# Optimization experiments

Hardware: AMD Instinct MI355X
Metric: run time of the kernel (lower is better)

The kernel has to match this reference:

```python
import jax, jax.numpy as jnp
import numpy as np

N_NODES = 100000
N_EDGES = 1600000
IN_DIM, HID_DIM, OUT_DIM = 512, 128, 64


def setup_inputs() -> dict:
    key = jax.random.key(0)
    k1, k2, k3, k4, k5, k6 = jax.random.split(key, 6)
    feature = jax.random.normal(k1, (N_NODES, IN_DIM), dtype=jnp.float32)
    edge_row = jax.random.randint(k2, (N_EDGES,), 0, N_NODES, dtype=jnp.int32)
    edge_col = jax.random.randint(k3, (N_EDGES,), 0, N_NODES, dtype=jnp.int32)
    edge_vals = jax.random.uniform(k4, (N_EDGES,), dtype=jnp.float32)
    W1 = jax.random.normal(k5, (IN_DIM, HID_DIM), dtype=jnp.float32) * (IN_DIM ** -0.5)
    W2 = jax.random.normal(k6, (HID_DIM, OUT_DIM), dtype=jnp.float32) * (HID_DIM ** -0.5)
    return {"feature": feature, "edge_row": edge_row, "edge_col": edge_col,
            "edge_vals": edge_vals, "W1": W1, "W2": W2}


def spmm(edge_row, edge_col, edge_vals, dense):
    # sparse [N,N] @ dense [N,D]: out[r] += v * dense[c] for each edge (r,c,v)
    gathered = edge_vals[:, None] * dense[edge_col]  # [E, D]
    return jax.ops.segment_sum(gathered, edge_row, num_segments=N_NODES)


def reference(feature, edge_row, edge_col, edge_vals, W1, W2):
    # layer 1: support = X @ W1; h = relu(A @ support)
    h = jax.nn.relu(spmm(edge_row, edge_col, edge_vals, feature @ W1))
    # layer 2: logits = A @ (h @ W2)
    logits = spmm(edge_row, edge_col, edge_vals, h @ W2)
    return logits
```

## Files before the change

### kernel.cpp

```cpp
#include <hip/hip_runtime.h>

#define N_NODES 100000
#define N_EDGES 1600000
#define IN_DIM 512
#define HID_DIM 128
#define OUT_DIM 64

typedef __attribute__((ext_vector_type(8))) short bf16x8;
typedef __attribute__((ext_vector_type(4))) float f32x4;

__device__ __forceinline__ unsigned int f2bf_rne(float f) {
    union { float f; unsigned u; } v; v.f = f;
    unsigned r = v.u + 0x7fffu + ((v.u >> 16) & 1u);
    return r >> 16;
}

__global__ __launch_bounds__(256) void wcvt(const float* __restrict__ W1,
                                            unsigned short* __restrict__ W1t) {
    __shared__ float T[64][65];
    const int bk = blockIdx.x >> 1;
    const int bn = blockIdx.x & 1;
    const int t = threadIdx.x;
#pragma unroll
    for (int i = 0; i < 4; i++) {
        int fi = t + i * 256;
        int kk = fi >> 4;
        int f  = fi & 15;
        float4 v = *(const float4*)&W1[(long)(bk * 64 + kk) * HID_DIM + bn * 64 + f * 4];
        T[kk][f * 4 + 0] = v.x; T[kk][f * 4 + 1] = v.y;
        T[kk][f * 4 + 2] = v.z; T[kk][f * 4 + 3] = v.w;
    }
    __syncthreads();
#pragma unroll
    for (int i = 0; i < 8; i++) {
        int di = t + i * 256;
        int n  = di >> 5;
        int dw = di & 31;
        unsigned lo = f2bf_rne(T[dw * 2 + 0][n]);
        unsigned hi = f2bf_rne(T[dw * 2 + 1][n]);
        unsigned short* dst = W1t + (long)(bn * 64 + n) * IN_DIM + bk * 64 + dw * 2;
        *(unsigned int*)dst = lo | (hi << 16);
    }
}

__global__ __launch_bounds__(256) void wcvt2(const float* __restrict__ W2,
                                             unsigned short* __restrict__ W2t) {
    __shared__ float T[128][65];
    const int t = threadIdx.x;
#pragma unroll
    for (int i = 0; i < 8; i++) {
        int fi = t + i * 256;
        int k = fi >> 4;
        int f = fi & 15;
        float4 v = *(const float4*)&W2[(long)k * OUT_DIM + f * 4];
        T[k][f * 4 + 0] = v.x; T[k][f * 4 + 1] = v.y;
        T[k][f * 4 + 2] = v.z; T[k][f * 4 + 3] = v.w;
    }
    __syncthreads();
#pragma unroll
    for (int i = 0; i < 16; i++) {
        int di = t + i * 256;
        int n  = di >> 6;
        int dw = di & 63;
        unsigned lo = f2bf_rne(T[dw * 2 + 0][n]);
        unsigned hi = f2bf_rne(T[dw * 2 + 1][n]);
        *(unsigned int*)(W2t + (long)n * HID_DIM + dw * 2) = lo | (hi << 16);
    }
}

__global__ __launch_bounds__(256) void gemm1_mfma(const float* __restrict__ X,
                                                  const unsigned short* __restrict__ W1t,
                                                  unsigned short* __restrict__ outb) {
    __shared__ unsigned short As[64][40];
    const int tid  = threadIdx.x;
    const int lane = tid & 63;
    const int w    = tid >> 6;
    const int m    = lane & 15;
    const int hi   = lane >> 4;
    const int rowBase = blockIdx.x * 64;

    f32x4 acc[4][2] = {};

    const int sr = tid >> 2;
    const int sk = (tid & 3) * 8;
    int gr = rowBase + sr;
    if (gr >= N_NODES) gr = N_NODES - 1;
    const float* xp = X + (long)gr * IN_DIM;

    const unsigned short* b0p = W1t + (long)(w * 32 + m) * IN_DIM + hi * 8;
    const unsigned short* b1p = W1t + (long)(w * 32 + 16 + m) * IN_DIM + hi * 8;

    for (int k0 = 0; k0 < IN_DIM; k0 += 32) {
        float4 xa = *(const float4*)(xp + k0 + sk);
        float4 xb = *(const float4*)(xp + k0 + sk + 4);
        uint4 pk;
        pk.x = f2bf_rne(xa.x) | (f2bf_rne(xa.y) << 16);
        pk.y = f2bf_rne(xa.z) | (f2bf_rne(xa.w) << 16);
        pk.z = f2bf_rne(xb.x) | (f2bf_rne(xb.y) << 16);
        pk.w = f2bf_rne(xb.z) | (f2bf_rne(xb.w) << 16);
        *(uint4*)&As[sr][sk] = pk;
        __syncthreads();

        bf16x8 bf0 = *(const bf16x8*)(b0p + k0);
        bf16x8 bf1 = *(const bf16x8*)(b1p + k0);
#pragma unroll
        for (int t = 0; t < 4; t++) {
            bf16x8 af = *(const bf16x8*)&As[t * 16 + m][hi * 8];
            acc[t][0] = __builtin_amdgcn_mfma_f32_16x16x32_bf16(af, bf0, acc[t][0], 0, 0, 0);
            acc[t][1] = __builtin_amdgcn_mfma_f32_16x16x32_bf16(af, bf1, acc[t][1], 0, 0, 0);
        }
        __syncthreads();
    }

#pragma unroll
    for (int t = 0; t < 4; t++) {
#pragma unroll
        for (int r = 0; r < 4; r++) {
            int row = rowBase + t * 16 + hi * 4 + r;
            if (row < N_NODES) {
                outb[(long)row * HID_DIM + w * 32 + m] =
                    (unsigned short)f2bf_rne(acc[t][0][r]);
                outb[(long)row * HID_DIM + w * 32 + 16 + m] =
                    (unsigned short)f2bf_rne(acc[t][1][r]);
            }
        }
    }
}

__global__ __launch_bounds__(256) void gemm2_mfma(const unsigned short* __restrict__ hb,
                                                  const unsigned short* __restrict__ W2t,
                                                  float* __restrict__ hw) {
    const int tid  = threadIdx.x;
    const int lane = tid & 63;
    const int w    = tid >> 6;
    const int m    = lane & 15;
    const int hi   = lane >> 4;
    const long rowBase = (long)blockIdx.x * 128 + w * 32;

    bf16x8 bfrag[4][4];
#pragma unroll
    for (int nt = 0; nt < 4; nt++) {
        const unsigned short* bp = W2t + (long)(nt * 16 + m) * HID_DIM + hi * 8;
#pragma unroll
        for (int ks = 0; ks < 4; ks++)
            bfrag[ks][nt] = *(const bf16x8*)(bp + ks * 32);
    }

    f32x4 acc[2][4] = {};
#pragma unroll
    for (int mt = 0; mt < 2; mt++) {
        long r = rowBase + mt * 16 + m;
        if (r >= N_NODES) r = N_NODES - 1;
        const unsigned short* ap = hb + r * HID_DIM + hi * 8;
#pragma unroll
        for (int ks = 0; ks < 4; ks++) {
            bf16x8 af = *(const bf16x8*)(ap + ks * 32);
#pragma unroll
            for (int nt = 0; nt < 4; nt++)
                acc[mt][nt] = __builtin_amdgcn_mfma_f32_16x16x32_bf16(
                    af, bfrag[ks][nt], acc[mt][nt], 0, 0, 0);
        }
    }

#pragma unroll
    for (int mt = 0; mt < 2; mt++)
#pragma unroll
        for (int nt = 0; nt < 4; nt++)
#pragma unroll
            for (int r = 0; r < 4; r++) {
                long row = rowBase + mt * 16 + hi * 4 + r;
                if (row < N_NODES)
                    hw[row * OUT_DIM + nt * 16 + m] = acc[mt][nt][r];
            }
}

__global__ __launch_bounds__(256) void hist_rows(const int* __restrict__ rows,
                                                 int* __restrict__ cnt) {
    int e = blockIdx.x * 256 + threadIdx.x;
    if (e < N_EDGES) atomicAdd(&cnt[rows[e]], 1);
}

#define SCAN_BLOCKS ((N_NODES + 255) / 256)

__global__ __launch_bounds__(256) void scan_pass1(int* __restrict__ cnt,
                                                  int* __restrict__ bsum) {
    __shared__ int s[256];
    const int t = threadIdx.x;
    const int i = blockIdx.x * 256 + t;
    int v = (i < N_NODES) ? cnt[i] : 0;
    s[t] = v;
    __syncthreads();
    for (int off = 1; off < 256; off <<= 1) {
        int u = (t >= off) ? s[t - off] : 0;
        __syncthreads();
        s[t] += u;
        __syncthreads();
    }
    if (i < N_NODES) cnt[i] = s[t] - v;
    if (t == 255) bsum[blockIdx.x] = s[255];
}

__global__ __launch_bounds__(512) void scan_pass2(int* __restrict__ bsum,
                                                  int* __restrict__ boff) {
    __shared__ int s[512];
    const int t = threadIdx.x;
    int v = (t < SCAN_BLOCKS) ? bsum[t] : 0;
    s[t] = v;
    __syncthreads();
    for (int off = 1; off < 512; off <<= 1) {
        int u = (t >= off) ? s[t - off] : 0;
        __syncthreads();
        s[t] += u;
        __syncthreads();
    }
    if (t < SCAN_BLOCKS) boff[t] = s[t] - v;
}

__global__ __launch_bounds__(256) void scan_pass3(const int* __restrict__ cnt,
                                                  const int* __restrict__ boff,
                                                  int* __restrict__ rowptr,
                                                  int* __restrict__ cursor) {
    const int i = blockIdx.x * 256 + threadIdx.x;
    if (i < N_NODES) {
        int r = cnt[i] + boff[blockIdx.x];
        rowptr[i] = r;
        cursor[i] = r;
    }
    if (i == 0) rowptr[N_NODES] = N_EDGES;
}

__global__ __launch_bounds__(256) void scatter_edges(const int* __restrict__ rows,
                                                     const int* __restrict__ cols,
                                                     const float* __restrict__ vals,
                                                     int* __restrict__ cursor,
                                                     int2* __restrict__ sedge) {
    int e = blockIdx.x * 256 + threadIdx.x;
    if (e < N_EDGES) {
        int p = atomicAdd(&cursor[rows[e]], 1);
        sedge[p] = make_int2(cols[e], __float_as_int(vals[e]));
    }
}

__global__ __launch_bounds__(256) void spmm1(const int* __restrict__ rowptr,
                                             const int2* __restrict__ sedge,
                                             const unsigned short* __restrict__ supb,
                                             unsigned short* __restrict__ outb) {
    const int wid = blockIdx.x * 4 + (threadIdx.x >> 6);
    if (wid >= N_NODES) return;
    const int lane = threadIdx.x & 63;
    const int start = rowptr[wid];
    const int end   = rowptr[wid + 1];

    float accx = 0.f, accy = 0.f;

    for (int base = start; base < end; base += 64) {
        int idx = base + lane;
        int ecol = 0, eval = 0;
        if (idx < end) {
            int2 e = sedge[idx];
            ecol = e.x; eval = e.y;
        }
        const int cnt = min(64, end - base);
        for (int k = 0; k < cnt; k += 8) {
            int   c[8];
            float v[8];
#pragma unroll
            for (int q = 0; q < 8; q++) {
                c[q] = __builtin_amdgcn_readlane(ecol, k + q);
                v[q] = __int_as_float(__builtin_amdgcn_readlane(eval, k + q));
            }
            unsigned u[8];
#pragma unroll
            for (int q = 0; q < 8; q++)
                u[q] = *(const unsigned*)(supb + (long)c[q] * 128 + lane * 2);
#pragma unroll
            for (int q = 0; q < 8; q++) {
                accx += v[q] * __uint_as_float(u[q] << 16);
                accy += v[q] * __uint_as_float(u[q] & 0xffff0000u);
            }
        }
    }

    accx = accx > 0.f ? accx : 0.f;
    accy = accy > 0.f ? accy : 0.f;
    *(unsigned int*)(outb + (long)wid * 128 + lane * 2) =
        f2bf_rne(accx) | (f2bf_rne(accy) << 16);
}

__global__ __launch_bounds__(256) void spmm2(const int* __restrict__ rowptr,
                                             const int2* __restrict__ sedge,
                                             const float* __restrict__ dense,
                                             float* __restrict__ out) {
    const int wid = blockIdx.x * 4 + (threadIdx.x >> 6);
    if (wid >= N_NODES) return;
    const int lane = threadIdx.x & 63;
    const int start = rowptr[wid];
    const int end   = rowptr[wid + 1];

    float acc = 0.f;

    for (int base = start; base < end; base += 64) {
        int idx = base + lane;
        int ecol = 0, eval = 0;
        if (idx < end) {
            int2 e = sedge[idx];
            ecol = e.x; eval = e.y;
        }
        const int cnt = min(64, end - base);
        for (int k = 0; k < cnt; k += 8) {
            int   c[8];
            float v[8];
#pragma unroll
            for (int q = 0; q < 8; q++) {
                c[q] = __builtin_amdgcn_readlane(ecol, k + q);
                v[q] = __int_as_float(__builtin_amdgcn_readlane(eval, k + q));
            }
            float x[8];
#pragma unroll
            for (int q = 0; q < 8; q++)
                x[q] = dense[(long)c[q] * 64 + lane];
#pragma unroll
            for (int q = 0; q < 8; q++)
                acc += v[q] * x[q];
        }
    }

    out[(long)wid * 64 + lane] = acc;
}

extern "C" void kernel_launch(void* const* d_in, const int* in_sizes, int n_in,
                              void* d_out, int out_size, void* d_ws, size_t ws_size,
                              hipStream_t stream) {
    const float* feature = (const float*)d_in[0];
    const int*   erow    = (const int*)d_in[1];
    const int*   ecol    = (const int*)d_in[2];
    const float* evals   = (const float*)d_in[3];
    const float* W1      = (const float*)d_in[4];
    const float* W2      = (const float*)d_in[5];
    float* out = (float*)d_out;

    unsigned short* supb = (unsigned short*)d_ws;
    unsigned short* hb   = supb + (size_t)N_NODES * HID_DIM;
    float* hw      = (float*)(hb + (size_t)N_NODES * HID_DIM);
    int*   cnt     = (int*)(hw + (size_t)N_NODES * OUT_DIM);
    int*   cursor  = cnt + N_NODES;
    int*   rowptr  = cursor + N_NODES;
    int2*  sedge   = (int2*)(rowptr + (N_NODES + 1));
    int*   bsum    = (int*)(sedge + N_EDGES);
    int*   boff    = bsum + SCAN_BLOCKS;
    unsigned short* W1t = (unsigned short*)(boff + SCAN_BLOCKS);
    unsigned short* W2t = W1t + (size_t)HID_DIM * IN_DIM;

    hipMemsetAsync(cnt, 0, (size_t)N_NODES * sizeof(int), stream);
    hist_rows<<<(N_EDGES + 255) / 256, 256, 0, stream>>>(erow, cnt);
    scan_pass1<<<SCAN_BLOCKS, 256, 0, stream>>>(cnt, bsum);
    scan_pass2<<<1, 512, 0, stream>>>(bsum, boff);
    scan_pass3<<<SCAN_BLOCKS, 256, 0, stream>>>(cnt, boff, rowptr, cursor);
    scatter_edges<<<(N_EDGES + 255) / 256, 256, 0, stream>>>(erow, ecol, evals,
                                                             cursor, sedge);

    wcvt<<<16, 256, 0, stream>>>(W1, W1t);
    wcvt2<<<1, 256, 0, stream>>>(W2, W2t);

    gemm1_mfma<<<(N_NODES + 63) / 64, 256, 0, stream>>>(feature, W1t, supb);

    spmm1<<<(N_NODES + 3) / 4, 256, 0, stream>>>(rowptr, sedge, supb, hb);

    gemm2_mfma<<<(N_NODES + 127) / 128, 256, 0, stream>>>(hb, W2t, hw);

    spmm2<<<(N_NODES + 3) / 4, 256, 0, stream>>>(rowptr, sedge, hw, out);
}
```

Baseline: 643.5 us.

## Partition CSR build atomics by XCD row range and widen SpMM gather batches

The histogram and scatter kernels now use a fixed grid where each block's low three index bits pick one of eight row ranges. Each block scans all edges but only does atomics for rows in its range, so atomic traffic for a row range stays on one XCD's L2 rather than spreading across dies. The cost is that every edge's row index is read eight times, using nontemporal loads. Separately, both SpMM kernels unroll the neighbor gather to 16 edges per batch instead of 8, which puts more loads in flight at the cost of more registers.

```diff
diff --git a/kernel.cpp b/kernel.cpp
--- a/kernel.cpp
+++ b/kernel.cpp
@@ -174,10 +174,20 @@
             }
 }
 
-__global__ __launch_bounds__(256) void hist_rows(const int* __restrict__ rows,
-                                                 int* __restrict__ cnt) {
-    int e = blockIdx.x * 256 + threadIdx.x;
-    if (e < N_EDGES) atomicAdd(&cnt[rows[e]], 1);
+#define ROWS_PER_GRP (N_NODES / 8)
+#define CSR_BLOCKS 1024
+
+__global__ __launch_bounds__(256) void hist_xcd(const int* __restrict__ rows,
+                                                int* __restrict__ cnt) {
+    const int grp = blockIdx.x & 7;
+    const int rlo = grp * ROWS_PER_GRP;
+    const int rhi = rlo + ROWS_PER_GRP;
+    const int nb  = gridDim.x >> 3;
+    const int bi  = blockIdx.x >> 3;
+    for (int e = bi * 256 + threadIdx.x; e < N_EDGES; e += nb * 256) {
+        int r = __builtin_nontemporal_load(&rows[e]);
+        if (r >= rlo && r < rhi) atomicAdd(&cnt[r], 1);
+    }
 }
 
 #define SCAN_BLOCKS ((N_NODES + 255) / 256)
@@ -229,15 +239,24 @@
     if (i == 0) rowptr[N_NODES] = N_EDGES;
 }
 
-__global__ __launch_bounds__(256) void scatter_edges(const int* __restrict__ rows,
-                                                     const int* __restrict__ cols,
-                                                     const float* __restrict__ vals,
-                                                     int* __restrict__ cursor,
-                                                     int2* __restrict__ sedge) {
-    int e = blockIdx.x * 256 + threadIdx.x;
-    if (e < N_EDGES) {
-        int p = atomicAdd(&cursor[rows[e]], 1);
-        sedge[p] = make_int2(cols[e], __float_as_int(vals[e]));
+__global__ __launch_bounds__(256) void scatter_xcd(const int* __restrict__ rows,
+                                                   const int* __restrict__ cols,
+                                                   const float* __restrict__ vals,
+                                                   int* __restrict__ cursor,
+                                                   int2* __restrict__ sedge) {
+    const int grp = blockIdx.x & 7;
+    const int rlo = grp * ROWS_PER_GRP;
+    const int rhi = rlo + ROWS_PER_GRP;
+    const int nb  = gridDim.x >> 3;
+    const int bi  = blockIdx.x >> 3;
+    for (int e = bi * 256 + threadIdx.x; e < N_EDGES; e += nb * 256) {
+        int r = __builtin_nontemporal_load(&rows[e]);
+        if (r >= rlo && r < rhi) {
+            int   c = __builtin_nontemporal_load(&cols[e]);
+            float v = __builtin_nontemporal_load(&vals[e]);
+            int p = atomicAdd(&cursor[r], 1);
+            sedge[p] = make_int2(c, __float_as_int(v));
+        }
     }
 }
 
@@ -261,20 +280,20 @@
             ecol = e.x; eval = e.y;
         }
         const int cnt = min(64, end - base);
-        for (int k = 0; k < cnt; k += 8) {
-            int   c[8];
-            float v[8];
-#pragma unroll
-            for (int q = 0; q < 8; q++) {
+        for (int k = 0; k < cnt; k += 16) {
+            int   c[16];
+            float v[16];
+#pragma unroll
+            for (int q = 0; q < 16; q++) {
                 c[q] = __builtin_amdgcn_readlane(ecol, k + q);
                 v[q] = __int_as_float(__builtin_amdgcn_readlane(eval, k + q));
             }
-            unsigned u[8];
-#pragma unroll
-            for (int q = 0; q < 8; q++)
+            unsigned u[16];
+#pragma unroll
+            for (int q = 0; q < 16; q++)
                 u[q] = *(const unsigned*)(supb + (long)c[q] * 128 + lane * 2);
 #pragma unroll
-            for (int q = 0; q < 8; q++) {
+            for (int q = 0; q < 16; q++) {
                 accx += v[q] * __uint_as_float(u[q] << 16);
                 accy += v[q] * __uint_as_float(u[q] & 0xffff0000u);
             }
@@ -307,20 +326,20 @@
             ecol = e.x; eval = e.y;
         }
         const int cnt = min(64, end - base);
-        for (int k = 0; k < cnt; k += 8) {
-            int   c[8];
-            float v[8];
-#pragma unroll
-            for (int q = 0; q < 8; q++) {
+        for (int k = 0; k < cnt; k += 16) {
+            int   c[16];
+            float v[16];
+#pragma unroll
+            for (int q = 0; q < 16; q++) {
                 c[q] = __builtin_amdgcn_readlane(ecol, k + q);
                 v[q] = __int_as_float(__builtin_amdgcn_readlane(eval, k + q));
             }
-            float x[8];
-#pragma unroll
-            for (int q = 0; q < 8; q++)
+            float x[16];
+#pragma unroll
+            for (int q = 0; q < 16; q++)
                 x[q] = dense[(long)c[q] * 64 + lane];
 #pragma unroll
-            for (int q = 0; q < 8; q++)
+            for (int q = 0; q < 16; q++)
                 acc += v[q] * x[q];
         }
     }
@@ -352,12 +371,11 @@
     unsigned short* W2t = W1t + (size_t)HID_DIM * IN_DIM;
 
     hipMemsetAsync(cnt, 0, (size_t)N_NODES * sizeof(int), stream);
-    hist_rows<<<(N_EDGES + 255) / 256, 256, 0, stream>>>(erow, cnt);
+    hist_xcd<<<CSR_BLOCKS, 256, 0, stream>>>(erow, cnt);
     scan_pass1<<<SCAN_BLOCKS, 256, 0, stream>>>(cnt, bsum);
     scan_pass2<<<1, 512, 0, stream>>>(bsum, boff);
     scan_pass3<<<SCAN_BLOCKS, 256, 0, stream>>>(cnt, boff, rowptr, cursor);
-    scatter_edges<<<(N_EDGES + 255) / 256, 256, 0, stream>>>(erow, ecol, evals,
-                                                             cursor, sedge);
+    scatter_xcd<<<CSR_BLOCKS, 256, 0, stream>>>(erow, ecol, evals, cursor, sedge);
 
     wcvt<<<16, 256, 0, stream>>>(W1, W1t);
     wcvt2<<<1, 256, 0, stream>>>(W2, W2t);
```

New measurement: 606.3 us. 5.8% less time.
